# Performance work log

Hardware: AMD Instinct MI355X
Metric: run time of the kernel (lower is better)

## Reference

```python
import jax, jax.numpy as jnp
import numpy as np

B, N, DIM = 2, 2048, 2048
H, DK, DV = 16, 64, 128
DIM_INNER = (DK + DV) * H  # 3072
EPS = 1e-12  # matches F.normalize clamp_min eps


def l2norm(t):
    n = jnp.linalg.norm(t, axis=-1, keepdims=True)
    return t / jnp.maximum(n, EPS)


def tanh_norm(t):
    n = jnp.linalg.norm(t, axis=-1, keepdims=True)
    return jnp.tanh(n) * (t / jnp.maximum(n, EPS))


def setup_inputs() -> dict:
    key = jax.random.key(0)
    k1, k2, k3, k4 = jax.random.split(key, 4)
    tokens = jax.random.normal(k1, (B, N, DIM), dtype=jnp.float32)
    # Linear weights stored as [in, out] (y = x @ W)
    Wqg = jax.random.normal(k2, (DIM, DIM_INNER), dtype=jnp.float32) * (DIM ** -0.5)
    Wkv = jax.random.normal(k3, (DIM, DIM_INNER), dtype=jnp.float32) * (DIM ** -0.5)
    Wo = jax.random.normal(k4, (DV * H, DIM), dtype=jnp.float32) * ((DV * H) ** -0.5)
    # LearnedScale log_scales, init log(1.0) = 0
    ls_iaw = jnp.zeros((H,), dtype=jnp.float32)  # inverse_acceptance_width (bias=1.0)
    ls_hws = jnp.zeros((H,), dtype=jnp.float32)  # head_wise_scale (bias=0.0)
    return {"tokens": tokens, "Wqg": Wqg, "Wkv": Wkv, "Wo": Wo,
            "ls_iaw": ls_iaw, "ls_hws": ls_hws}


def _split_heads(t):
    # [b, n, h*d] -> [b, h, n, d]
    b, n, _ = t.shape
    return t.reshape(b, n, H, -1).transpose(0, 2, 1, 3)


def reference(tokens, Wqg, Wkv, Wo, ls_iaw, ls_hws):
    qg = _split_heads(tokens @ Wqg)   # [b, h, n, dk+dv]
    kv = _split_heads(tokens @ Wkv)
    queries, gates = qg[..., :DK], qg[..., DK:]
    keys, values = kv[..., :DK], kv[..., DK:]
    queries, keys, values = l2norm(queries), l2norm(keys), l2norm(values)

    sim = jnp.einsum('bhid,bhjd->bhij', queries, keys)
    # r = 1 / (exp(log_scales) + 1)  (LearnedScale bias=1.0)
    r = 1.0 / (jnp.exp(ls_iaw) + 1.0)[None, :, None, None]
    attn = jnp.square(jax.nn.relu(1.0 - r * (1.0 - sim)))
    # NOTE: original code applies causal mask to `sim` AFTER computing `attn`,
    # so the mask has no effect on the output -- replicated faithfully here.
    aggr = jnp.einsum('bhij,bhjd->bhid', attn, values)
    out = tanh_norm(aggr) * jnp.tanh(jax.nn.silu(gates))
    out = out * jnp.exp(ls_hws)[None, :, None, None]  # head_wise_scale, bias=0
    out = out.transpose(0, 2, 1, 3).reshape(tokens.shape[0], tokens.shape[1], H * DV)
    return out @ Wo
```

## Files before the change

kernel.cpp:

```cpp
#include <hip/hip_runtime.h>
#include <hip/hip_bf16.h>
#include <stdint.h>


typedef unsigned short u16;
typedef __bf16 bf16x8 __attribute__((ext_vector_type(8)));
typedef u16 u16x8 __attribute__((ext_vector_type(8)));
typedef float f32x4 __attribute__((ext_vector_type(4)));

#define DEVINL __device__ __forceinline__

DEVINL u16 f2bf(float f) {
  union { float f; uint32_t u; } v; v.f = f;
  uint32_t r = (v.u + 0x7FFFu + ((v.u >> 16) & 1u)) >> 16;
  return (u16)r;
}
DEVINL float bf2f(u16 x) {
  union { uint32_t u; float f; } v; v.u = ((uint32_t)x) << 16;
  return v.f;
}
DEVINL bf16x8 as_bf(u16x8 v) { return __builtin_bit_cast(bf16x8, v); }

typedef const __attribute__((address_space(1))) uint32_t* gptr_t;
typedef __attribute__((address_space(3))) uint32_t* lptr_t;
DEVINL void gload_lds16(const void* g, void* l) {
  __builtin_amdgcn_global_load_lds((gptr_t)g, (lptr_t)l, 16, 0, 0);
}

DEVINL f32x4 mfma16(u16x8 a, u16x8 b, f32x4 c) {
  return __builtin_amdgcn_mfma_f32_16x16x32_bf16(as_bf(a), as_bf(b), c, 0, 0, 0);
}

__global__ void k_cvt(const float* __restrict__ src, u16* __restrict__ dst, int n) {
  int i = (blockIdx.x * blockDim.x + threadIdx.x) * 4;
  int stride = gridDim.x * blockDim.x * 4;
  for (; i < n; i += stride) {
    float4 f = *(const float4*)(src + i);
    ushort4 o;
    o.x = f2bf(f.x); o.y = f2bf(f.y); o.z = f2bf(f.z); o.w = f2bf(f.w);
    *(ushort4*)(dst + i) = o;
  }
}

__global__ void k_cvtT(const float* __restrict__ src, u16* __restrict__ dst, int R, int C) {
  __shared__ float tile[32][33];
  int c0 = blockIdx.x * 32, r0 = blockIdx.y * 32;
  int tc = threadIdx.x & 31, tr = threadIdx.x >> 5;
#pragma unroll
  for (int i = 0; i < 4; i++) {
    int r = tr + i * 8;
    tile[r][tc] = src[(size_t)(r0 + r) * C + c0 + tc];
  }
  __syncthreads();
#pragma unroll
  for (int i = 0; i < 4; i++) {
    int r = tr + i * 8;
    dst[(size_t)(c0 + r) * R + r0 + tc] = f2bf(tile[tc][r]);
  }
}

template <int F32OUT>
__global__ __launch_bounds__(256, 2) void k_gemm(const u16* __restrict__ A,
                                                 const u16* __restrict__ Bt,
                                                 void* __restrict__ Cout,
                                                 int M, int Nt, int K) {
  __shared__ u16 As[128 * 32];
  __shared__ u16 Bs[128 * 32];
  const int tid = threadIdx.x, lane = tid & 63, wid = tid >> 6;
  const int m0 = blockIdx.y * 128, n0 = blockIdx.x * 128;
  const int wm = (wid >> 1) * 64, wn = (wid & 1) * 64;
  const int fr = lane & 15, fc = (lane >> 4) * 8;

  f32x4 acc[4][4] = {};

  const u16* gA = A + (size_t)(m0 + wid * 32 + (lane >> 2)) * K + (lane & 3) * 8;
  const u16* gB = Bt + (size_t)(n0 + wid * 32 + (lane >> 2)) * K + (lane & 3) * 8;
  u16* lA = As + wid * 1024;
  u16* lB = Bs + wid * 1024;
  const size_t rowskip = (size_t)16 * K;

  for (int k0 = 0; k0 < K; k0 += 32) {
    gload_lds16(gA + k0, lA);
    gload_lds16(gA + k0 + rowskip, lA + 512);
    gload_lds16(gB + k0, lB);
    gload_lds16(gB + k0 + rowskip, lB + 512);
    __syncthreads();
    u16x8 a[4], b[4];
#pragma unroll
    for (int mi = 0; mi < 4; mi++) a[mi] = *(const u16x8*)(As + (wm + mi * 16 + fr) * 32 + fc);
#pragma unroll
    for (int ni = 0; ni < 4; ni++) b[ni] = *(const u16x8*)(Bs + (wn + ni * 16 + fr) * 32 + fc);
#pragma unroll
    for (int mi = 0; mi < 4; mi++)
#pragma unroll
      for (int ni = 0; ni < 4; ni++)
        acc[mi][ni] = mfma16(a[mi], b[ni], acc[mi][ni]);
    __syncthreads();
  }

  const int frow = (lane >> 4) * 4;
#pragma unroll
  for (int mi = 0; mi < 4; mi++)
#pragma unroll
    for (int ni = 0; ni < 4; ni++)
#pragma unroll
      for (int j = 0; j < 4; j++) {
        const size_t row = m0 + wm + mi * 16 + frow + j;
        const size_t col = n0 + wn + ni * 16 + fr;
        if (F32OUT) ((float*)Cout)[row * Nt + col] = acc[mi][ni][j];
        else ((u16*)Cout)[row * Nt + col] = f2bf(acc[mi][ni][j]);
      }
}

__global__ __launch_bounds__(256, 4) void k_norm(const u16* __restrict__ qg,
                                                 const u16* __restrict__ kv,
                                                 u16* __restrict__ qn, u16* __restrict__ kn,
                                                 u16* __restrict__ vnT, u16* __restrict__ gact) {
  __shared__ u16 vt[128 * 64];
  const int tid = threadIdx.x, lane = tid & 63, wid = tid >> 6;
  const int hb = blockIdx.y;
  const int h = hb & 15, b = hb >> 4;
  const int n0 = blockIdx.x * 64;

  for (int s = 0; s < 16; s++) {
    const int nl = wid * 16 + s;
    const int n = n0 + nl;
    const size_t bn = (size_t)b * 2048 + n;
    const size_t base = bn * 3072 + (size_t)h * 192;

    float q = bf2f(qg[base + lane]);
    float g0 = bf2f(qg[base + 64 + lane]);
    float g1 = bf2f(qg[base + 128 + lane]);
    float k = bf2f(kv[base + lane]);
    float v0 = bf2f(kv[base + 64 + lane]);
    float v1 = bf2f(kv[base + 128 + lane]);

    float qs = q * q, ks = k * k, vs = v0 * v0 + v1 * v1;
#pragma unroll
    for (int m = 1; m < 64; m <<= 1) {
      qs += __shfl_xor(qs, m);
      ks += __shfl_xor(ks, m);
      vs += __shfl_xor(vs, m);
    }
    float rq = 1.f / fmaxf(sqrtf(qs), 1e-12f);
    float rk = 1.f / fmaxf(sqrtf(ks), 1e-12f);
    float rv = 1.f / fmaxf(sqrtf(vs), 1e-12f);

    qn[((size_t)hb * 2048 + n) * 64 + lane] = f2bf(q * rq);
    kn[((size_t)hb * 2048 + n) * 64 + lane] = f2bf(k * rk);
    float s0 = g0 / (1.f + __expf(-g0));
    float s1 = g1 / (1.f + __expf(-g1));
    gact[((size_t)hb * 2048 + n) * 128 + lane] = f2bf(tanhf(s0));
    gact[((size_t)hb * 2048 + n) * 128 + 64 + lane] = f2bf(tanhf(s1));

    const int d0 = lane, d1 = 64 + lane;
    vt[d0 * 64 + (nl ^ ((d0 & 15) << 2))] = f2bf(v0 * rv);
    vt[d1 * 64 + (nl ^ ((d1 & 15) << 2))] = f2bf(v1 * rv);
  }
  __syncthreads();

#pragma unroll
  for (int p = 0; p < 8; p++) {
    const int d = p * 16 + (tid >> 4);
    const int nq = (tid & 15) * 4;
    const int cb = nq ^ ((d & 15) << 2);
    ushort4 o;
    o.x = vt[d * 64 + cb + 0];
    o.y = vt[d * 64 + cb + 1];
    o.z = vt[d * 64 + cb + 2];
    o.w = vt[d * 64 + cb + 3];
    *(ushort4*)(vnT + ((size_t)hb * 128 + d) * 2048 + n0 + nq) = o;
  }
}

__global__ __launch_bounds__(256, 2) void k_attn(const u16* __restrict__ qn,
                                                 const u16* __restrict__ kn,
                                                 const u16* __restrict__ vnT,
                                                 const u16* __restrict__ gact,
                                                 const float* __restrict__ ls_iaw,
                                                 const float* __restrict__ ls_hws,
                                                 u16* __restrict__ pre_out) {
  extern __shared__ char smem[];
  u16* KsB = (u16*)smem;
  u16* VsB = (u16*)(smem + 16384);
  u16* Ps = (u16*)(smem + 49152);
  float* nbuf = (float*)(smem + 49152);

  const int tid = threadIdx.x, lane = tid & 63, wid = tid >> 6;
  const int bh = blockIdx.y, h = bh & 15;
  const int n0 = blockIdx.x * 128;
  const int wq = (wid >> 1) * 64;
  const int wckv = (wid & 1) * 32;
  const int wcd = (wid & 1) * 64;
  const float r = 1.f / (__expf(ls_iaw[h]) + 1.f);
  const float whs = __expf(ls_hws[h]);
  const int fr = lane & 15, hi = lane >> 4, fc = hi * 8, frow = hi * 4;
  const int rb = fr & 7;

  const u16* qbase = qn + ((size_t)bh * 2048 + n0) * 64;
  u16x8 qf[4][2];
#pragma unroll
  for (int mi = 0; mi < 4; mi++)
#pragma unroll
    for (int kk = 0; kk < 2; kk++)
      qf[mi][kk] = *(const u16x8*)(qbase + (wq + mi * 16 + fr) * 64 + kk * 32 + fc);

  f32x4 acc[4][4] = {};
  const u16* kbase = kn + (size_t)bh * 2048 * 64;
  const u16* vbase = vnT + (size_t)bh * 128 * 2048;

  int ks_goff[2];
#pragma unroll
  for (int i = 0; i < 2; i++) {
    int row = wid * 16 + i * 8 + (lane >> 3);
    ks_goff[i] = row * 64 + (((lane & 7) ^ (row & 7)) << 3);
  }
  int vs_goff[4];
#pragma unroll
  for (int i = 0; i < 4; i++) {
    int row = wid * 32 + i * 8 + (lane >> 3);
    vs_goff[i] = row * 2048 + (((lane & 7) ^ (row & 7)) << 3);
  }

  {
    u16* KsC = KsB + wid * 1024;
    u16* VsC = VsB + wid * 2048;
#pragma unroll
    for (int i = 0; i < 2; i++) gload_lds16(kbase + ks_goff[i], KsC + i * 512);
#pragma unroll
    for (int i = 0; i < 4; i++) gload_lds16(vbase + vs_goff[i], VsC + i * 512);
  }

  int cur = 0;
  for (int t = 0; t < 32; t++) {
    asm volatile("s_waitcnt vmcnt(0) lgkmcnt(0)" ::: "memory");
    __builtin_amdgcn_s_barrier();
    asm volatile("" ::: "memory");

    if (t < 31) {
      const int kv0 = (t + 1) * 64;
      u16* KsC2 = KsB + (cur ^ 1) * 4096 + wid * 1024;
      u16* VsC2 = VsB + (cur ^ 1) * 8192 + wid * 2048;
#pragma unroll
      for (int i = 0; i < 2; i++) gload_lds16(kbase + (size_t)kv0 * 64 + ks_goff[i], KsC2 + i * 512);
#pragma unroll
      for (int i = 0; i < 4; i++) gload_lds16(vbase + (size_t)vs_goff[i] + kv0, VsC2 + i * 512);
    }

    const u16* KsC = KsB + cur * 4096;
    f32x4 s[4][2] = {};
    __builtin_amdgcn_s_setprio(1);
#pragma unroll
    for (int kk = 0; kk < 2; kk++) {
      u16x8 kf[2];
#pragma unroll
      for (int ni = 0; ni < 2; ni++) {
        const int row = wckv + ni * 16 + fr;
        kf[ni] = *(const u16x8*)(KsC + row * 64 + (((kk * 4 + hi) ^ rb) << 3));
      }
#pragma unroll
      for (int mi = 0; mi < 4; mi++)
#pragma unroll
        for (int ni = 0; ni < 2; ni++)
          s[mi][ni] = mfma16(qf[mi][kk], kf[ni], s[mi][ni]);
    }
    __builtin_amdgcn_s_setprio(0);

#pragma unroll
    for (int mi = 0; mi < 4; mi++)
#pragma unroll
      for (int ni = 0; ni < 2; ni++)
#pragma unroll
        for (int j = 0; j < 4; j++) {
          const int row = wq + mi * 16 + frow + j;
          const int col = wckv + ni * 16 + fr;
          float p = fmaxf(0.f, 1.f - r * (1.f - s[mi][ni][j]));
          Ps[row * 64 + (col ^ ((row & 7) << 3))] = f2bf(p * p);
        }

    asm volatile("s_waitcnt lgkmcnt(0)" ::: "memory");
    __builtin_amdgcn_s_barrier();
    asm volatile("" ::: "memory");

    const u16* VsC = VsB + cur * 8192;
    __builtin_amdgcn_s_setprio(1);
#pragma unroll
    for (int kk = 0; kk < 2; kk++) {
      u16x8 pf[4], vf[4];
#pragma unroll
      for (int mi = 0; mi < 4; mi++) {
        const int row = wq + mi * 16 + fr;
        pf[mi] = *(const u16x8*)(Ps + row * 64 + (((kk * 4 + hi) ^ rb) << 3));
      }
#pragma unroll
      for (int ni = 0; ni < 4; ni++) {
        const int row = wcd + ni * 16 + fr;
        vf[ni] = *(const u16x8*)(VsC + row * 64 + (((kk * 4 + hi) ^ rb) << 3));
      }
#pragma unroll
      for (int mi = 0; mi < 4; mi++)
#pragma unroll
        for (int ni = 0; ni < 4; ni++)
          acc[mi][ni] = mfma16(pf[mi], vf[ni], acc[mi][ni]);
    }
    __builtin_amdgcn_s_setprio(0);
    cur ^= 1;
  }
  __syncthreads();

#pragma unroll
  for (int mi = 0; mi < 4; mi++)
#pragma unroll
    for (int j = 0; j < 4; j++) {
      float ss = 0.f;
#pragma unroll
      for (int ni = 0; ni < 4; ni++) { float x = acc[mi][ni][j]; ss += x * x; }
#pragma unroll
      for (int m = 1; m < 16; m <<= 1) ss += __shfl_xor(ss, m);
      if (fr == 0) nbuf[(wid & 1) * 128 + wq + mi * 16 + frow + j] = ss;
    }
  __syncthreads();

  const size_t gbase = ((size_t)bh * 2048 + n0) * 128;
  const size_t obase = ((size_t)(bh >> 4) * 2048 + n0);
#pragma unroll
  for (int mi = 0; mi < 4; mi++)
#pragma unroll
    for (int j = 0; j < 4; j++) {
      const int row = wq + mi * 16 + frow + j;
      float nsq = nbuf[row] + nbuf[128 + row];
      float nn = sqrtf(nsq);
      float scale = tanhf(nn) / fmaxf(nn, 1e-12f) * whs;
#pragma unroll
      for (int ni = 0; ni < 4; ni++) {
        const int d = wcd + ni * 16 + fr;
        float gv = bf2f(gact[gbase + (size_t)row * 128 + d]);
        pre_out[(obase + row) * 2048 + h * 128 + d] = f2bf(acc[mi][ni][j] * scale * gv);
      }
    }
}

extern "C" void kernel_launch(void* const* d_in, const int* in_sizes, int n_in,
                              void* d_out, int out_size, void* d_ws, size_t ws_size,
                              hipStream_t stream) {
  (void)in_sizes; (void)n_in; (void)out_size; (void)ws_size;
  const float* tokens = (const float*)d_in[0];
  const float* Wqg = (const float*)d_in[1];
  const float* Wkv = (const float*)d_in[2];
  const float* Wo = (const float*)d_in[3];
  const float* ls_iaw = (const float*)d_in[4];
  const float* ls_hws = (const float*)d_in[5];
  float* out = (float*)d_out;
  char* ws = (char*)d_ws;

  u16* WoT = (u16*)(ws + 0);
  char* regA = ws + 8388608;
  u16* tok_bf = (u16*)(regA);
  u16* WqgT = (u16*)(regA + 16777216);
  u16* WkvT = (u16*)(regA + 29360128);
  u16* qn = (u16*)(regA);
  u16* kn = (u16*)(regA + 8388608);
  u16* vnT = (u16*)(regA + 16777216);
  u16* gact = (u16*)(regA + 33554432);
  char* regB = ws + 58720256;
  u16* qg_raw = (u16*)(regB);
  u16* kv_raw = (u16*)(regB + 25165824);
  u16* pre_out = (u16*)(regB);

  k_cvt<<<4096, 256, 0, stream>>>(tokens, tok_bf, 8388608);
  k_cvtT<<<dim3(96, 64), 256, 0, stream>>>(Wqg, WqgT, 2048, 3072);
  k_cvtT<<<dim3(96, 64), 256, 0, stream>>>(Wkv, WkvT, 2048, 3072);
  k_cvtT<<<dim3(64, 64), 256, 0, stream>>>(Wo, WoT, 2048, 2048);

  k_gemm<0><<<dim3(24, 32), 256, 0, stream>>>(tok_bf, WqgT, qg_raw, 4096, 3072, 2048);
  k_gemm<0><<<dim3(24, 32), 256, 0, stream>>>(tok_bf, WkvT, kv_raw, 4096, 3072, 2048);

  k_norm<<<dim3(32, 32), 256, 0, stream>>>(qg_raw, kv_raw, qn, kn, vnT, gact);

  k_attn<<<dim3(16, 32), 256, 65536, stream>>>(qn, kn, vnT, gact, ls_iaw, ls_hws, pre_out);

  k_gemm<1><<<dim3(16, 32), 256, 0, stream>>>(pre_out, WoT, out, 4096, 2048, 2048);
}
```

Measured before the change: 309.6 us.

## Rewrite attention with 32x32 MFMA register-resident P and fuse QG/KV projections

The attention kernel moves from 16x16x32 to 32x32x16 MFMAs and computes the transposed score tile. This lets the squared-relu weights be packed straight into registers as the B operand of the PV product, removing the LDS round-trip for P and one barrier per KV tile. The vT layout written by the norm kernel is permuted to match the new operand order. The output norm becomes a per-lane reduction, and the result is staged through LDS for coalesced stores. The two projection GEMMs are merged into one wider GEMM over a concatenated weight, and the attention grid is remapped over blocks; the extra index logic adds some risk of layout mismatch.

```diff
diff --git a/kernel.cpp b/kernel.cpp
--- a/kernel.cpp
+++ b/kernel.cpp
@@ -7,6 +7,8 @@
 typedef __bf16 bf16x8 __attribute__((ext_vector_type(8)));
 typedef u16 u16x8 __attribute__((ext_vector_type(8)));
 typedef float f32x4 __attribute__((ext_vector_type(4)));
+typedef float f32x16 __attribute__((ext_vector_type(16)));
+typedef int i32x4 __attribute__((ext_vector_type(4)));
 
 #define DEVINL __device__ __forceinline__
 
@@ -29,6 +31,9 @@
 
 DEVINL f32x4 mfma16(u16x8 a, u16x8 b, f32x4 c) {
   return __builtin_amdgcn_mfma_f32_16x16x32_bf16(as_bf(a), as_bf(b), c, 0, 0, 0);
+}
+DEVINL f32x16 mfma32(u16x8 a, u16x8 b, f32x16 c) {
+  return __builtin_amdgcn_mfma_f32_32x32x16_bf16(as_bf(a), as_bf(b), c, 0, 0, 0);
 }
 
 __global__ void k_cvt(const float* __restrict__ src, u16* __restrict__ dst, int n) {
@@ -112,8 +117,7 @@
       }
 }
 
-__global__ __launch_bounds__(256, 4) void k_norm(const u16* __restrict__ qg,
-                                                 const u16* __restrict__ kv,
+__global__ __launch_bounds__(256, 4) void k_norm(const u16* __restrict__ qgkv,
                                                  u16* __restrict__ qn, u16* __restrict__ kn,
                                                  u16* __restrict__ vnT, u16* __restrict__ gact) {
   __shared__ u16 vt[128 * 64];
@@ -126,14 +130,15 @@
     const int nl = wid * 16 + s;
     const int n = n0 + nl;
     const size_t bn = (size_t)b * 2048 + n;
-    const size_t base = bn * 3072 + (size_t)h * 192;
-
-    float q = bf2f(qg[base + lane]);
-    float g0 = bf2f(qg[base + 64 + lane]);
-    float g1 = bf2f(qg[base + 128 + lane]);
-    float k = bf2f(kv[base + lane]);
-    float v0 = bf2f(kv[base + 64 + lane]);
-    float v1 = bf2f(kv[base + 128 + lane]);
+    const size_t baseq = bn * 6144 + (size_t)h * 192;
+    const size_t basek = baseq + 3072;
+
+    float q = bf2f(qgkv[baseq + lane]);
+    float g0 = bf2f(qgkv[baseq + 64 + lane]);
+    float g1 = bf2f(qgkv[baseq + 128 + lane]);
+    float k = bf2f(qgkv[basek + lane]);
+    float v0 = bf2f(qgkv[basek + 64 + lane]);
+    float v1 = bf2f(qgkv[basek + 128 + lane]);
 
     float qs = q * q, ks = k * k, vs = v0 * v0 + v1 * v1;
 #pragma unroll
@@ -164,12 +169,13 @@
     const int d = p * 16 + (tid >> 4);
     const int nq = (tid & 15) * 4;
     const int cb = nq ^ ((d & 15) << 2);
+    const int nq2 = (nq & ~12) | ((nq & 4) << 1) | ((nq & 8) >> 1);
     ushort4 o;
     o.x = vt[d * 64 + cb + 0];
     o.y = vt[d * 64 + cb + 1];
     o.z = vt[d * 64 + cb + 2];
     o.w = vt[d * 64 + cb + 3];
-    *(ushort4*)(vnT + ((size_t)hb * 128 + d) * 2048 + n0 + nq) = o;
+    *(ushort4*)(vnT + ((size_t)hb * 128 + d) * 2048 + n0 + nq2) = o;
   }
 }
 
@@ -183,29 +189,25 @@
   extern __shared__ char smem[];
   u16* KsB = (u16*)smem;
   u16* VsB = (u16*)(smem + 16384);
-  u16* Ps = (u16*)(smem + 49152);
-  float* nbuf = (float*)(smem + 49152);
+  u16* Os = (u16*)smem;
 
   const int tid = threadIdx.x, lane = tid & 63, wid = tid >> 6;
-  const int bh = blockIdx.y, h = bh & 15;
-  const int n0 = blockIdx.x * 128;
-  const int wq = (wid >> 1) * 64;
-  const int wckv = (wid & 1) * 32;
-  const int wcd = (wid & 1) * 64;
+  const int bid = blockIdx.y * 16 + blockIdx.x;
+  const int bh = (bid & 7) * 4 + ((bid >> 3) & 3);
+  const int n0 = (bid >> 5) * 128;
+  const int h = bh & 15;
+  const int l31 = lane & 31, L = lane >> 5, rb = l31 & 7;
   const float r = 1.f / (__expf(ls_iaw[h]) + 1.f);
+  const float c1 = 1.f - r;
   const float whs = __expf(ls_hws[h]);
-  const int fr = lane & 15, hi = lane >> 4, fc = hi * 8, frow = hi * 4;
-  const int rb = fr & 7;
-
-  const u16* qbase = qn + ((size_t)bh * 2048 + n0) * 64;
-  u16x8 qf[4][2];
-#pragma unroll
-  for (int mi = 0; mi < 4; mi++)
-#pragma unroll
-    for (int kk = 0; kk < 2; kk++)
-      qf[mi][kk] = *(const u16x8*)(qbase + (wq + mi * 16 + fr) * 64 + kk * 32 + fc);
-
-  f32x4 acc[4][4] = {};
+
+  const int wq = wid * 32;
+  const u16* qrow = qn + ((size_t)bh * 2048 + n0 + wq + l31) * 64;
+  u16x8 qf[4];
+#pragma unroll
+  for (int c = 0; c < 4; c++) qf[c] = *(const u16x8*)(qrow + c * 16 + L * 8);
+
+  f32x16 acc[4] = {};
   const u16* kbase = kn + (size_t)bh * 2048 * 64;
   const u16* vbase = vnT + (size_t)bh * 128 * 2048;
 
@@ -248,96 +250,89 @@
     }
 
     const u16* KsC = KsB + cur * 4096;
-    f32x4 s[4][2] = {};
+    const u16* VsC = VsB + cur * 8192;
+
+    f32x16 sT0 = {}, sT1 = {};
     __builtin_amdgcn_s_setprio(1);
 #pragma unroll
-    for (int kk = 0; kk < 2; kk++) {
-      u16x8 kf[2];
-#pragma unroll
-      for (int ni = 0; ni < 2; ni++) {
-        const int row = wckv + ni * 16 + fr;
-        kf[ni] = *(const u16x8*)(KsC + row * 64 + (((kk * 4 + hi) ^ rb) << 3));
-      }
-#pragma unroll
-      for (int mi = 0; mi < 4; mi++)
-#pragma unroll
-        for (int ni = 0; ni < 2; ni++)
-          s[mi][ni] = mfma16(qf[mi][kk], kf[ni], s[mi][ni]);
+    for (int c = 0; c < 4; c++) {
+      u16x8 kf0 = *(const u16x8*)(KsC + (0 + l31) * 64 + (((2 * c + L) ^ rb) << 3));
+      u16x8 kf1 = *(const u16x8*)(KsC + (32 + l31) * 64 + (((2 * c + L) ^ rb) << 3));
+      sT0 = mfma32(kf0, qf[c], sT0);
+      sT1 = mfma32(kf1, qf[c], sT1);
     }
     __builtin_amdgcn_s_setprio(0);
 
-#pragma unroll
-    for (int mi = 0; mi < 4; mi++)
-#pragma unroll
-      for (int ni = 0; ni < 2; ni++)
-#pragma unroll
-        for (int j = 0; j < 4; j++) {
-          const int row = wq + mi * 16 + frow + j;
-          const int col = wckv + ni * 16 + fr;
-          float p = fmaxf(0.f, 1.f - r * (1.f - s[mi][ni][j]));
-          Ps[row * 64 + (col ^ ((row & 7) << 3))] = f2bf(p * p);
+    uint32_t w[2][4][2];
+#pragma unroll
+    for (int m = 0; m < 4; m++)
+#pragma unroll
+      for (int p = 0; p < 2; p++) {
+        float a0 = fmaxf(0.f, fmaf(r, sT0[4 * m + 2 * p], c1));
+        float a1 = fmaxf(0.f, fmaf(r, sT0[4 * m + 2 * p + 1], c1));
+        float b0 = fmaxf(0.f, fmaf(r, sT1[4 * m + 2 * p], c1));
+        float b1 = fmaxf(0.f, fmaf(r, sT1[4 * m + 2 * p + 1], c1));
+        w[0][m][p] = (uint32_t)f2bf(a0 * a0) | ((uint32_t)f2bf(a1 * a1) << 16);
+        w[1][m][p] = (uint32_t)f2bf(b0 * b0) | ((uint32_t)f2bf(b1 * b1) << 16);
+      }
+
+    __builtin_amdgcn_s_setprio(1);
+#pragma unroll
+    for (int kt = 0; kt < 2; kt++)
+#pragma unroll
+      for (int pair = 0; pair < 2; pair++) {
+        i32x4 pw;
+        pw[0] = (int)w[kt][2 * pair][0];
+        pw[1] = (int)w[kt][2 * pair][1];
+        pw[2] = (int)w[kt][2 * pair + 1][0];
+        pw[3] = (int)w[kt][2 * pair + 1][1];
+        u16x8 pf = __builtin_bit_cast(u16x8, pw);
+        const int chunk = 4 * kt + 2 * pair + L;
+#pragma unroll
+        for (int dt = 0; dt < 4; dt++) {
+          u16x8 vf = *(const u16x8*)(VsC + (dt * 32 + l31) * 64 + ((chunk ^ rb) << 3));
+          acc[dt] = mfma32(vf, pf, acc[dt]);
         }
-
-    asm volatile("s_waitcnt lgkmcnt(0)" ::: "memory");
-    __builtin_amdgcn_s_barrier();
-    asm volatile("" ::: "memory");
-
-    const u16* VsC = VsB + cur * 8192;
-    __builtin_amdgcn_s_setprio(1);
-#pragma unroll
-    for (int kk = 0; kk < 2; kk++) {
-      u16x8 pf[4], vf[4];
-#pragma unroll
-      for (int mi = 0; mi < 4; mi++) {
-        const int row = wq + mi * 16 + fr;
-        pf[mi] = *(const u16x8*)(Ps + row * 64 + (((kk * 4 + hi) ^ rb) << 3));
       }
-#pragma unroll
-      for (int ni = 0; ni < 4; ni++) {
-        const int row = wcd + ni * 16 + fr;
-        vf[ni] = *(const u16x8*)(VsC + row * 64 + (((kk * 4 + hi) ^ rb) << 3));
-      }
-#pragma unroll
-      for (int mi = 0; mi < 4; mi++)
-#pragma unroll
-        for (int ni = 0; ni < 4; ni++)
-          acc[mi][ni] = mfma16(pf[mi], vf[ni], acc[mi][ni]);
-    }
     __builtin_amdgcn_s_setprio(0);
     cur ^= 1;
   }
+
+  float ss = 0.f;
+#pragma unroll
+  for (int dt = 0; dt < 4; dt++)
+#pragma unroll
+    for (int e = 0; e < 16; e++) { float x = acc[dt][e]; ss += x * x; }
+  ss += __shfl_xor(ss, 32);
+  float nn = sqrtf(ss);
+  float scale = tanhf(nn) / fmaxf(nn, 1e-12f) * whs;
+
   __syncthreads();
 
-#pragma unroll
-  for (int mi = 0; mi < 4; mi++)
-#pragma unroll
-    for (int j = 0; j < 4; j++) {
-      float ss = 0.f;
-#pragma unroll
-      for (int ni = 0; ni < 4; ni++) { float x = acc[mi][ni][j]; ss += x * x; }
-#pragma unroll
-      for (int m = 1; m < 16; m <<= 1) ss += __shfl_xor(ss, m);
-      if (fr == 0) nbuf[(wid & 1) * 128 + wq + mi * 16 + frow + j] = ss;
+  const int q = wq + l31;
+  const size_t grow = ((size_t)bh * 2048 + n0 + q) * 128;
+#pragma unroll
+  for (int dt = 0; dt < 4; dt++)
+#pragma unroll
+    for (int m = 0; m < 4; m++) {
+      const int d = dt * 32 + 8 * m + 4 * L;
+      ushort4 gv = *(const ushort4*)(gact + grow + d);
+      ushort4 o;
+      o.x = f2bf(acc[dt][4 * m + 0] * scale * bf2f(gv.x));
+      o.y = f2bf(acc[dt][4 * m + 1] * scale * bf2f(gv.y));
+      o.z = f2bf(acc[dt][4 * m + 2] * scale * bf2f(gv.z));
+      o.w = f2bf(acc[dt][4 * m + 3] * scale * bf2f(gv.w));
+      *(ushort4*)(Os + q * 132 + d) = o;
     }
   __syncthreads();
 
-  const size_t gbase = ((size_t)bh * 2048 + n0) * 128;
-  const size_t obase = ((size_t)(bh >> 4) * 2048 + n0);
-#pragma unroll
-  for (int mi = 0; mi < 4; mi++)
-#pragma unroll
-    for (int j = 0; j < 4; j++) {
-      const int row = wq + mi * 16 + frow + j;
-      float nsq = nbuf[row] + nbuf[128 + row];
-      float nn = sqrtf(nsq);
-      float scale = tanhf(nn) / fmaxf(nn, 1e-12f) * whs;
-#pragma unroll
-      for (int ni = 0; ni < 4; ni++) {
-        const int d = wcd + ni * 16 + fr;
-        float gv = bf2f(gact[gbase + (size_t)row * 128 + d]);
-        pre_out[(obase + row) * 2048 + h * 128 + d] = f2bf(acc[mi][ni][j] * scale * gv);
-      }
-    }
+  const int orow = tid >> 1, oc0 = (tid & 1) * 64;
+  const size_t obase = ((size_t)(bh >> 4) * 2048 + n0 + orow) * 2048 + (size_t)h * 128 + oc0;
+#pragma unroll
+  for (int j = 0; j < 16; j++) {
+    ushort4 v = *(const ushort4*)(Os + orow * 132 + oc0 + 4 * j);
+    *(ushort4*)(pre_out + obase + 4 * j) = v;
+  }
 }
 
 extern "C" void kernel_launch(void* const* d_in, const int* in_sizes, int n_in,
@@ -356,28 +351,25 @@
   u16* WoT = (u16*)(ws + 0);
   char* regA = ws + 8388608;
   u16* tok_bf = (u16*)(regA);
-  u16* WqgT = (u16*)(regA + 16777216);
-  u16* WkvT = (u16*)(regA + 29360128);
+  u16* WqgkvT = (u16*)(regA + 16777216);
   u16* qn = (u16*)(regA);
   u16* kn = (u16*)(regA + 8388608);
   u16* vnT = (u16*)(regA + 16777216);
   u16* gact = (u16*)(regA + 33554432);
   char* regB = ws + 58720256;
-  u16* qg_raw = (u16*)(regB);
-  u16* kv_raw = (u16*)(regB + 25165824);
+  u16* qgkv_raw = (u16*)(regB);
   u16* pre_out = (u16*)(regB);
 
   k_cvt<<<4096, 256, 0, stream>>>(tokens, tok_bf, 8388608);
-  k_cvtT<<<dim3(96, 64), 256, 0, stream>>>(Wqg, WqgT, 2048, 3072);
-  k_cvtT<<<dim3(96, 64), 256, 0, stream>>>(Wkv, WkvT, 2048, 3072);
+  k_cvtT<<<dim3(96, 64), 256, 0, stream>>>(Wqg, WqgkvT, 2048, 3072);
+  k_cvtT<<<dim3(96, 64), 256, 0, stream>>>(Wkv, WqgkvT + (size_t)3072 * 2048, 2048, 3072);
   k_cvtT<<<dim3(64, 64), 256, 0, stream>>>(Wo, WoT, 2048, 2048);
 
-  k_gemm<0><<<dim3(24, 32), 256, 0, stream>>>(tok_bf, WqgT, qg_raw, 4096, 3072, 2048);
-  k_gemm<0><<<dim3(24, 32), 256, 0, stream>>>(tok_bf, WkvT, kv_raw, 4096, 3072, 2048);
-
-  k_norm<<<dim3(32, 32), 256, 0, stream>>>(qg_raw, kv_raw, qn, kn, vnT, gact);
-
-  k_attn<<<dim3(16, 32), 256, 65536, stream>>>(qn, kn, vnT, gact, ls_iaw, ls_hws, pre_out);
+  k_gemm<0><<<dim3(48, 32), 256, 0, stream>>>(tok_bf, WqgkvT, qgkv_raw, 4096, 6144, 2048);
+
+  k_norm<<<dim3(32, 32), 256, 0, stream>>>(qgkv_raw, qn, kn, vnT, gact);
+
+  k_attn<<<dim3(16, 32), 256, 49152, stream>>>(qn, kn, vnT, gact, ls_iaw, ls_hws, pre_out);
 
   k_gemm<1><<<dim3(16, 32), 256, 0, stream>>>(pre_out, WoT, out, 4096, 2048, 2048);
 }
```

New measurement: 302.1 us. -2.4%, faster.
